# Performance work log

Hardware: AMD Instinct MI355X
Metric: run time of the kernel (lower is better)

The kernel has to match this reference:

```python
import jax, jax.numpy as jnp
import numpy as np

NUM_BITS = 10
MEM_SIZE = 2 ** NUM_BITS  # 1024
HIDDEN = 1024
INPUT = 1024
BATCH = 16384
LN_EPS = 1e-5


def setup_inputs() -> dict:
    key = jax.random.key(0)
    ks = jax.random.split(key, 8)
    s = 0.02
    return {
        "x": jax.random.normal(ks[0], (BATCH, INPUT), jnp.float32),
        "h_prev": jax.random.normal(ks[1], (BATCH, HIDDEN), jnp.float32),
        "memory": jax.random.normal(ks[2], (MEM_SIZE, HIDDEN), jnp.float32),
        "W_w": jax.random.normal(ks[3], (HIDDEN, INPUT), jnp.float32) * s,
        "W_b": jnp.zeros((HIDDEN,), jnp.float32),
        "U_w": jax.random.normal(ks[4], (HIDDEN, HIDDEN), jnp.float32) * s,
        "U_b": jnp.zeros((HIDDEN,), jnp.float32),
        "Q_w": jax.random.normal(ks[5], (HIDDEN, HIDDEN), jnp.float32) * s,
        "Q_b": jnp.zeros((HIDDEN,), jnp.float32),
        "M_w": jax.random.normal(ks[6], (NUM_BITS, HIDDEN), jnp.float32) * s,
        "M_b": jnp.zeros((NUM_BITS,), jnp.float32),
        "ln_g": jnp.ones((HIDDEN,), jnp.float32),
        "ln_b": jnp.zeros((HIDDEN,), jnp.float32),
    }


def reference(x, h_prev, memory, W_w, W_b, U_w, U_b, Q_w, Q_b, M_w, M_b, ln_g, ln_b):
    # Binary address from h_prev (eval-mode hard threshold, non-differentiable)
    powers = jnp.asarray(2 ** np.arange(NUM_BITS - 1, -1, -1), dtype=x.dtype)  # [num_bits]
    logits = h_prev @ M_w.T + M_b                              # [B, num_bits]
    binary = (jax.nn.sigmoid(logits) > 0.5).astype(x.dtype)    # hard bits
    index = jnp.clip((binary * powers).sum(-1).astype(jnp.int32), 0, MEM_SIZE - 1)  # [B]
    h_mem = memory[index]                                      # gather [B, H]
    # Fused linear combine + LayerNorm + sigmoid
    pre = x @ W_w.T + W_b + h_prev @ U_w.T + U_b + h_mem @ Q_w.T + Q_b  # [B, H]
    mu = pre.mean(-1, keepdims=True)
    var = ((pre - mu) ** 2).mean(-1, keepdims=True)            # biased var (torch LN)
    norm = (pre - mu) * jax.lax.rsqrt(var + LN_EPS)
    return jax.nn.sigmoid(norm * ln_g + ln_b)                  # h_new [B, H]
```

## Files before the change

kernel.cpp:

```cpp
#include <hip/hip_runtime.h>

#define BATCH   16384
#define HIDDEN  1024
#define K2      2048
#define MEMSZ   1024
#define NBITS   10

#define BM 256
#define BN 256
#define BK 64
#define NT (K2 / BK)

typedef __bf16 bf16x8 __attribute__((ext_vector_type(8)));
typedef float  f32x4  __attribute__((ext_vector_type(4)));

__device__ __forceinline__ unsigned short f2bf(float f) {
    unsigned int u = __float_as_uint(f);
    u += 0x7FFFu + ((u >> 16) & 1u);
    return (unsigned short)(u >> 16);
}

__device__ __forceinline__ void gload_lds16(const void* g, void* l) {
    __builtin_amdgcn_global_load_lds(
        (const __attribute__((address_space(1))) unsigned int*)g,
        (__attribute__((address_space(3))) unsigned int*)l,
        16, 0, 0);
}

__global__ void pack_kernel(const float* __restrict__ W,
                            const float* __restrict__ U,
                            const float* __restrict__ memory,
                            const float* __restrict__ Q,
                            unsigned short* __restrict__ Bm,
                            unsigned short* __restrict__ Mem,
                            unsigned short* __restrict__ Qb) {
    int u = blockIdx.x * 256 + threadIdx.x;
    const float* src;
    unsigned short* dst;
    if (u < 524288) {
        int n = u >> 9;
        int k = (u & 511) * 4;
        src = (k < 1024) ? (W + (size_t)n * 1024 + k)
                         : (U + (size_t)n * 1024 + (k - 1024));
        dst = Bm + (size_t)n * K2 + k;
    } else if (u < 786432) {
        int f = (u - 524288) * 4;
        src = memory + f;  dst = Mem + f;
    } else if (u < 1048576) {
        int f = (u - 786432) * 4;
        src = Q + f;  dst = Qb + f;
    } else return;
    float4 v = *reinterpret_cast<const float4*>(src);
    ushort4 o;
    o.x = f2bf(v.x); o.y = f2bf(v.y); o.z = f2bf(v.z); o.w = f2bf(v.w);
    *reinterpret_cast<ushort4*>(dst) = o;
}

__global__ __launch_bounds__(256) void mq_kernel(
        const unsigned short* __restrict__ Mem,
        const unsigned short* __restrict__ Qb,
        float* __restrict__ MQ) {
    __shared__ unsigned short As[128 * 64];
    __shared__ unsigned short Bs[128 * 64];

    const int ks = blockIdx.x >> 6;
    const int mb = (blockIdx.x >> 3) & 7;
    const int nb = blockIdx.x & 7;
    const int t    = threadIdx.x;
    const int lane = t & 63;
    const int w    = t >> 6;
    const int wr   = w >> 1, wc = w & 1;
    const int rr   = lane & 15, rq = lane >> 4;
    const int c8   = (t & 7) * 8;
    const int srow = t >> 3;

    f32x4 acc[4][4] = {};

    for (int kt = 0; kt < 4; ++kt) {
        const int k0 = ks * 256 + kt * 64;
#pragma unroll
        for (int i = 0; i < 4; ++i) {
            int r = i * 32 + srow;
            gload_lds16(Mem + (size_t)(mb * 128 + r) * 1024 + k0 + c8, As + i * 2048 + t * 8);
            gload_lds16(Qb  + (size_t)(nb * 128 + r) * 1024 + k0 + c8, Bs + i * 2048 + t * 8);
        }
        __syncthreads();
#pragma unroll
        for (int kk = 0; kk < 2; ++kk) {
            const int krd = kk * 32 + rq * 8;
            bf16x8 af[4], bfv[4];
#pragma unroll
            for (int m = 0; m < 4; ++m)
                af[m] = *reinterpret_cast<const bf16x8*>(As + (wr * 64 + m * 16 + rr) * 64 + krd);
#pragma unroll
            for (int n = 0; n < 4; ++n)
                bfv[n] = *reinterpret_cast<const bf16x8*>(Bs + (wc * 64 + n * 16 + rr) * 64 + krd);
#pragma unroll
            for (int m = 0; m < 4; ++m)
#pragma unroll
                for (int n = 0; n < 4; ++n)
                    acc[m][n] = __builtin_amdgcn_mfma_f32_16x16x32_bf16(
                        af[m], bfv[n], acc[m][n], 0, 0, 0);
        }
        __syncthreads();
    }

#pragma unroll
    for (int m = 0; m < 4; ++m)
#pragma unroll
        for (int n = 0; n < 4; ++n) {
            int gcol = nb * 128 + wc * 64 + n * 16 + rr;
#pragma unroll
            for (int j = 0; j < 4; ++j) {
                int grow = mb * 128 + wr * 64 + m * 16 + rq * 4 + j;
                atomicAdd(&MQ[(size_t)grow * 1024 + gcol], acc[m][n][j]);
            }
        }
}

__global__ __launch_bounds__(256) void build_a_kernel(
        const float* __restrict__ x,
        const float* __restrict__ h_prev,
        const float* __restrict__ M_w,
        const float* __restrict__ M_b,
        unsigned short* __restrict__ A,
        int* __restrict__ idxbuf) {
    int row  = (blockIdx.x * blockDim.x + threadIdx.x) >> 6;
    int lane = threadIdx.x & 63;
    if (row >= BATCH) return;

    const float4* hp = reinterpret_cast<const float4*>(h_prev + (size_t)row * HIDDEN);
    float4 hv[4];
#pragma unroll
    for (int i = 0; i < 4; ++i) hv[i] = hp[i * 64 + lane];

    int idx = 0;
#pragma unroll
    for (int j = 0; j < NBITS; ++j) {
        const float4* mp = reinterpret_cast<const float4*>(M_w + (size_t)j * HIDDEN);
        float s = 0.f;
#pragma unroll
        for (int i = 0; i < 4; ++i) {
            float4 m = mp[i * 64 + lane];
            s += hv[i].x * m.x + hv[i].y * m.y + hv[i].z * m.z + hv[i].w * m.w;
        }
#pragma unroll
        for (int off = 32; off >= 1; off >>= 1) s += __shfl_xor(s, off, 64);
        float logit = s + M_b[j];
        if (logit > 0.f) idx |= (1 << (NBITS - 1 - j));
    }
    if (lane == 0) idxbuf[row] = idx;

    unsigned short* arow = A + (size_t)row * K2;
    const float4* xp = reinterpret_cast<const float4*>(x + (size_t)row * HIDDEN);
#pragma unroll
    for (int i = 0; i < 4; ++i) {
        int off = i * 256 + lane * 4;
        float4 vx = xp[i * 64 + lane];
        ushort4 ox; ox.x = f2bf(vx.x); ox.y = f2bf(vx.y); ox.z = f2bf(vx.z); ox.w = f2bf(vx.w);
        *reinterpret_cast<ushort4*>(arow + off) = ox;

        ushort4 oh; oh.x = f2bf(hv[i].x); oh.y = f2bf(hv[i].y); oh.z = f2bf(hv[i].z); oh.w = f2bf(hv[i].w);
        *reinterpret_cast<ushort4*>(arow + 1024 + off) = oh;
    }
}


__device__ __forceinline__ void stage_g(const unsigned short* __restrict__ src,
                                        int rowbase, int kt, int g,
                                        unsigned short* ldsTile, int t) {
    const int o      = g * 8192 + t * 16;
    const int row    = o >> 7;
    const int inner  = o & 127;
    const int sinner = inner ^ ((row & 7) << 4);
    const char* gp = reinterpret_cast<const char*>(
                         src + (size_t)(rowbase + row) * K2 + kt * BK) + sinner;
    gload_lds16(gp, reinterpret_cast<char*>(ldsTile) + o);
}

__device__ __forceinline__ bf16x8 ldsfrag(const unsigned short* tile, int row,
                                          int kbyte_x_sw) {
    return *reinterpret_cast<const bf16x8*>(
        reinterpret_cast<const char*>(tile) + row * 128 + kbyte_x_sw);
}

#define WAIT_PH(N)                                                   \
    do {                                                             \
        asm volatile("" ::: "memory");                               \
        __builtin_amdgcn_s_barrier();                                \
        asm volatile("s_waitcnt lgkmcnt(" #N ")" ::: "memory");      \
        __builtin_amdgcn_sched_barrier(0);                           \
    } while (0)

#define BAR_OUT()                                                    \
    do {                                                             \
        __builtin_amdgcn_sched_barrier(0);                           \
        asm volatile("" ::: "memory");                               \
        __builtin_amdgcn_s_barrier();                                \
    } while (0)

#define MFMA_Q(AF, MB, NB)                                                     \
    {                                                                          \
        __builtin_amdgcn_s_setprio(1);                                         \
        _Pragma("unroll") for (int m_ = 0; m_ < 4; ++m_)                       \
        _Pragma("unroll") for (int n_ = 0; n_ < 2; ++n_)                       \
        _Pragma("unroll") for (int kk_ = 0; kk_ < 2; ++kk_)                    \
            acc[(MB) + m_][(NB) + n_] =                                        \
                __builtin_amdgcn_mfma_f32_16x16x32_bf16(                       \
                    AF[m_][kk_], bfr[(NB) + n_][kk_],                          \
                    acc[(MB) + m_][(NB) + n_], 0, 0, 0);                       \
        __builtin_amdgcn_s_setprio(0);                                         \
    }

__global__ __launch_bounds__(512, 2) void gemm_kernel(
        const unsigned short* __restrict__ A,
        const unsigned short* __restrict__ Bm,
        float* __restrict__ C) {
    __shared__ alignas(16) unsigned short lds[2][2][BM * BK];

    const int bid  = blockIdx.x;
    const int wgid = (bid & 7) * 32 + (bid >> 3);
    const int mblk = wgid >> 2;
    const int nblk = wgid & 3;

    const int t    = threadIdx.x;
    const int lane = t & 63;
    const int w    = t >> 6;
    const int wr   = w >> 2;
    const int wc   = w & 3;
    const int rr   = lane & 15;
    const int rq   = lane >> 4;
    const int sw   = (rr & 7) << 4;
    const int rqb  = rq * 16;
    const int wrb  = wr * 128;
    const int wcb  = wc * 64;

    const int arow = mblk * BM;
    const int brow = nblk * BN;

    f32x4 acc[8][4] = {};

    {
#pragma unroll
        for (int g = 0; g < 4; ++g) stage_g(A,  arow, 0, g, &lds[0][0][0], t);
#pragma unroll
        for (int g = 0; g < 4; ++g) stage_g(Bm, brow, 0, g, &lds[0][1][0], t);
#pragma unroll
        for (int g = 0; g < 4; ++g) stage_g(Bm, brow, 1, g, &lds[1][1][0], t);
#pragma unroll
        for (int g = 0; g < 2; ++g) stage_g(A,  arow, 1, g, &lds[1][0][0], t);
        asm volatile("s_waitcnt vmcnt(6)" ::: "memory");
        asm volatile("" ::: "memory");
        __builtin_amdgcn_s_barrier();
    }

    bf16x8 af [4][2];
    bf16x8 af2[4][2];
    bf16x8 bfr[4][2];

#pragma unroll
    for (int m = 0; m < 4; ++m) {
        af[m][0] = ldsfrag(&lds[0][0][0], wrb + m * 16 + rr, (rqb) ^ sw);
        af[m][1] = ldsfrag(&lds[0][0][0], wrb + m * 16 + rr, (64 + rqb) ^ sw);
    }
#pragma unroll
    for (int n = 0; n < 2; ++n) {
        bfr[n][0] = ldsfrag(&lds[0][1][0], wcb + n * 16 + rr, (rqb) ^ sw);
        bfr[n][1] = ldsfrag(&lds[0][1][0], wcb + n * 16 + rr, (64 + rqb) ^ sw);
    }

    for (int kt = 0; kt < NT; ++kt) {
        const int c = kt & 1;
        const unsigned short* At = &lds[c][0][0];
        const unsigned short* Bt = &lds[c][1][0];
        const unsigned short* nxA = &lds[c ^ 1][0][0];
        const unsigned short* nxB = &lds[c ^ 1][1][0];
        unsigned short* curA = &lds[c][0][0];
        unsigned short* curB = &lds[c][1][0];
        const bool pf1 = (kt + 1 < NT);
        const bool pf2 = (kt + 2 < NT);

#pragma unroll
        for (int n = 2; n < 4; ++n) {
            bfr[n][0] = ldsfrag(Bt, wcb + n * 16 + rr, (rqb) ^ sw);
            bfr[n][1] = ldsfrag(Bt, wcb + n * 16 + rr, (64 + rqb) ^ sw);
        }
        if (pf1) {
            stage_g(A, arow, kt + 1, 2, (unsigned short*)nxA, t);
            stage_g(A, arow, kt + 1, 3, (unsigned short*)nxA, t);
        }
        WAIT_PH(4);
        MFMA_Q(af, 0, 0);
        BAR_OUT();

#pragma unroll
        for (int m = 0; m < 4; ++m) {
            af2[m][0] = ldsfrag(At, wrb + 64 + m * 16 + rr, (rqb) ^ sw);
            af2[m][1] = ldsfrag(At, wrb + 64 + m * 16 + rr, (64 + rqb) ^ sw);
        }
        WAIT_PH(8);
        MFMA_Q(af, 0, 2);
        BAR_OUT();

        if (pf2) {
            stage_g(Bm, brow, kt + 2, 0, curB, t);
            stage_g(Bm, brow, kt + 2, 1, curB, t);
        }
        WAIT_PH(0);
        MFMA_Q(af2, 4, 0);
        __builtin_amdgcn_sched_barrier(0);
        if (kt < NT - 2) {
            asm volatile("s_waitcnt vmcnt(2)" ::: "memory");
        } else if (kt == NT - 2) {
            asm volatile("s_waitcnt vmcnt(0)" ::: "memory");
        }
        asm volatile("" ::: "memory");
        __builtin_amdgcn_s_barrier();

        if (pf1) {
#pragma unroll
            for (int m = 0; m < 4; ++m) {
                af[m][0] = ldsfrag(nxA, wrb + m * 16 + rr, (rqb) ^ sw);
                af[m][1] = ldsfrag(nxA, wrb + m * 16 + rr, (64 + rqb) ^ sw);
            }
#pragma unroll
            for (int n = 0; n < 2; ++n) {
                bfr[n][0] = ldsfrag(nxB, wcb + n * 16 + rr, (rqb) ^ sw);
                bfr[n][1] = ldsfrag(nxB, wcb + n * 16 + rr, (64 + rqb) ^ sw);
            }
        }
        if (pf2) {
            stage_g(Bm, brow, kt + 2, 2, curB, t);
            stage_g(Bm, brow, kt + 2, 3, curB, t);
            stage_g(A,  arow, kt + 2, 0, curA, t);
            stage_g(A,  arow, kt + 2, 1, curA, t);
        }
        if (pf1) { WAIT_PH(12); } else { WAIT_PH(0); }
        MFMA_Q(af2, 4, 2);
        BAR_OUT();
    }

#pragma unroll
    for (int mi = 0; mi < 8; ++mi) {
#pragma unroll
        for (int n = 0; n < 4; ++n) {
            const int gcol = nblk * BN + wcb + n * 16 + rr;
#pragma unroll
            for (int j = 0; j < 4; ++j) {
                const int grow = mblk * BM + wrb + mi * 16 + rq * 4 + j;
                C[(size_t)grow * HIDDEN + gcol] = acc[mi][n][j];
            }
        }
    }
}

__global__ __launch_bounds__(256) void ln_kernel(
        float* __restrict__ C,
        const int* __restrict__ idxbuf,
        const float* __restrict__ MQ,
        const float* __restrict__ W_b, const float* __restrict__ U_b,
        const float* __restrict__ Q_b, const float* __restrict__ ln_g,
        const float* __restrict__ ln_b) {
    const int row = blockIdx.x;
    const int t   = threadIdx.x;
    const int midx = idxbuf[row];
    float4* rowp = reinterpret_cast<float4*>(C + (size_t)row * HIDDEN);
    const float4* mqp = reinterpret_cast<const float4*>(MQ + (size_t)midx * HIDDEN);

    float4 p  = rowp[t];
    float4 mq = mqp[t];
    float4 bw = reinterpret_cast<const float4*>(W_b)[t];
    float4 bu = reinterpret_cast<const float4*>(U_b)[t];
    float4 bq = reinterpret_cast<const float4*>(Q_b)[t];
    p.x += mq.x + bw.x + bu.x + bq.x;
    p.y += mq.y + bw.y + bu.y + bq.y;
    p.z += mq.z + bw.z + bu.z + bq.z;
    p.w += mq.w + bw.w + bu.w + bq.w;

    float s  = p.x + p.y + p.z + p.w;
    float sq = p.x * p.x + p.y * p.y + p.z * p.z + p.w * p.w;
#pragma unroll
    for (int off = 32; off >= 1; off >>= 1) {
        s  += __shfl_xor(s,  off, 64);
        sq += __shfl_xor(sq, off, 64);
    }
    __shared__ float red[8];
    const int lane = t & 63, w = t >> 6;
    if (lane == 0) { red[w] = s; red[4 + w] = sq; }
    __syncthreads();
    const float S    = red[0] + red[1] + red[2] + red[3];
    const float SQ   = red[4] + red[5] + red[6] + red[7];
    const float mean = S * (1.0f / HIDDEN);
    const float var  = SQ * (1.0f / HIDDEN) - mean * mean;
    const float rstd = rsqrtf(var + 1e-5f);

    float4 g = reinterpret_cast<const float4*>(ln_g)[t];
    float4 b = reinterpret_cast<const float4*>(ln_b)[t];
    float4 o;
    o.x = 1.f / (1.f + __expf(-((p.x - mean) * rstd * g.x + b.x)));
    o.y = 1.f / (1.f + __expf(-((p.y - mean) * rstd * g.y + b.y)));
    o.z = 1.f / (1.f + __expf(-((p.z - mean) * rstd * g.z + b.z)));
    o.w = 1.f / (1.f + __expf(-((p.w - mean) * rstd * g.w + b.w)));
    rowp[t] = o;
}

extern "C" void kernel_launch(void* const* d_in, const int* in_sizes, int n_in,
                              void* d_out, int out_size, void* d_ws, size_t ws_size,
                              hipStream_t stream) {
    const float* x      = (const float*)d_in[0];
    const float* h_prev = (const float*)d_in[1];
    const float* memory = (const float*)d_in[2];
    const float* W_w    = (const float*)d_in[3];
    const float* W_b    = (const float*)d_in[4];
    const float* U_w    = (const float*)d_in[5];
    const float* U_b    = (const float*)d_in[6];
    const float* Q_w    = (const float*)d_in[7];
    const float* Q_b    = (const float*)d_in[8];
    const float* M_w    = (const float*)d_in[9];
    const float* M_b    = (const float*)d_in[10];
    const float* ln_g   = (const float*)d_in[11];
    const float* ln_b   = (const float*)d_in[12];

    char* ws = (char*)d_ws;
    unsigned short* A   = (unsigned short*)(ws);
    unsigned short* Bm  = (unsigned short*)(ws + 67108864);
    unsigned short* Mem = (unsigned short*)(ws + 71303168);
    unsigned short* Qb  = (unsigned short*)(ws + 73400320);
    float*          MQ  = (float*)         (ws + 75497472);
    int*            idx = (int*)           (ws + 79691776);
    float* pre = (float*)d_out;

    hipLaunchKernelGGL(pack_kernel, dim3(4096), dim3(256), 0, stream,
                       W_w, U_w, memory, Q_w, Bm, Mem, Qb);
    hipMemsetAsync(MQ, 0, (size_t)MEMSZ * HIDDEN * sizeof(float), stream);
    hipLaunchKernelGGL(mq_kernel, dim3(256), dim3(256), 0, stream,
                       Mem, Qb, MQ);
    hipLaunchKernelGGL(build_a_kernel, dim3(BATCH / 4), dim3(256), 0, stream,
                       x, h_prev, M_w, M_b, A, idx);
    hipLaunchKernelGGL(gemm_kernel, dim3((BATCH / BM) * (HIDDEN / BN)), dim3(512), 0, stream,
                       A, Bm, pre);
    hipLaunchKernelGGL(ln_kernel, dim3(BATCH), dim3(256), 0, stream,
                       pre, idx, MQ, W_b, U_b, Q_b, ln_g, ln_b);
}
```

Baseline: 170.2 us.

## Merge pack and build kernels; reschedule GEMM LDS prefetch and fragment loads

Fuses the weight-packing kernel and the A-building/address kernel into one launch, with block ranges selecting the role, removing a launch and letting the two phases overlap. Restructures the GEMM main loop so B fragments use two separate register sets and A fragment loads are spread across phases. Full B tiles are now staged early and full A tiles after the third MFMA quadrant, with waitcnt and barrier placement adjusted to match. This trades a different latency-hiding schedule and register pressure for fewer stalls, and risks vmcnt mismatches.

```diff
diff --git a/kernel.cpp b/kernel.cpp
--- a/kernel.cpp
+++ b/kernel.cpp
@@ -27,33 +27,76 @@
         16, 0, 0);
 }
 
-__global__ void pack_kernel(const float* __restrict__ W,
-                            const float* __restrict__ U,
-                            const float* __restrict__ memory,
-                            const float* __restrict__ Q,
-                            unsigned short* __restrict__ Bm,
-                            unsigned short* __restrict__ Mem,
-                            unsigned short* __restrict__ Qb) {
-    int u = blockIdx.x * 256 + threadIdx.x;
-    const float* src;
-    unsigned short* dst;
-    if (u < 524288) {
-        int n = u >> 9;
-        int k = (u & 511) * 4;
-        src = (k < 1024) ? (W + (size_t)n * 1024 + k)
-                         : (U + (size_t)n * 1024 + (k - 1024));
-        dst = Bm + (size_t)n * K2 + k;
-    } else if (u < 786432) {
-        int f = (u - 524288) * 4;
-        src = memory + f;  dst = Mem + f;
-    } else if (u < 1048576) {
-        int f = (u - 786432) * 4;
-        src = Q + f;  dst = Qb + f;
-    } else return;
-    float4 v = *reinterpret_cast<const float4*>(src);
-    ushort4 o;
-    o.x = f2bf(v.x); o.y = f2bf(v.y); o.z = f2bf(v.z); o.w = f2bf(v.w);
-    *reinterpret_cast<ushort4*>(dst) = o;
+__global__ __launch_bounds__(256) void pack_build_kernel(
+        const float* __restrict__ W, const float* __restrict__ U,
+        const float* __restrict__ memory, const float* __restrict__ Q,
+        const float* __restrict__ x, const float* __restrict__ h_prev,
+        const float* __restrict__ M_w, const float* __restrict__ M_b,
+        unsigned short* __restrict__ Bm, unsigned short* __restrict__ Mem,
+        unsigned short* __restrict__ Qb, unsigned short* __restrict__ A,
+        int* __restrict__ idxbuf) {
+    if (blockIdx.x < 4096) {
+        int u = blockIdx.x * 256 + threadIdx.x;
+        const float* src;
+        unsigned short* dst;
+        if (u < 524288) {
+            int n = u >> 9;
+            int k = (u & 511) * 4;
+            src = (k < 1024) ? (W + (size_t)n * 1024 + k)
+                             : (U + (size_t)n * 1024 + (k - 1024));
+            dst = Bm + (size_t)n * K2 + k;
+        } else if (u < 786432) {
+            int f = (u - 524288) * 4;
+            src = memory + f;  dst = Mem + f;
+        } else {
+            int f = (u - 786432) * 4;
+            src = Q + f;  dst = Qb + f;
+        }
+        float4 v = *reinterpret_cast<const float4*>(src);
+        ushort4 o;
+        o.x = f2bf(v.x); o.y = f2bf(v.y); o.z = f2bf(v.z); o.w = f2bf(v.w);
+        *reinterpret_cast<ushort4*>(dst) = o;
+        return;
+    }
+
+    int row  = ((blockIdx.x - 4096) * 256 + threadIdx.x) >> 6;
+    int lane = threadIdx.x & 63;
+    if (row >= BATCH) return;
+
+    const float4* hp = reinterpret_cast<const float4*>(h_prev + (size_t)row * HIDDEN);
+    float4 hv[4];
+#pragma unroll
+    for (int i = 0; i < 4; ++i) hv[i] = hp[i * 64 + lane];
+
+    int idx = 0;
+#pragma unroll
+    for (int j = 0; j < NBITS; ++j) {
+        const float4* mp = reinterpret_cast<const float4*>(M_w + (size_t)j * HIDDEN);
+        float s = 0.f;
+#pragma unroll
+        for (int i = 0; i < 4; ++i) {
+            float4 m = mp[i * 64 + lane];
+            s += hv[i].x * m.x + hv[i].y * m.y + hv[i].z * m.z + hv[i].w * m.w;
+        }
+#pragma unroll
+        for (int off = 32; off >= 1; off >>= 1) s += __shfl_xor(s, off, 64);
+        float logit = s + M_b[j];
+        if (logit > 0.f) idx |= (1 << (NBITS - 1 - j));
+    }
+    if (lane == 0) idxbuf[row] = idx;
+
+    unsigned short* arow = A + (size_t)row * K2;
+    const float4* xp = reinterpret_cast<const float4*>(x + (size_t)row * HIDDEN);
+#pragma unroll
+    for (int i = 0; i < 4; ++i) {
+        int off = i * 256 + lane * 4;
+        float4 vx = xp[i * 64 + lane];
+        ushort4 ox; ox.x = f2bf(vx.x); ox.y = f2bf(vx.y); ox.z = f2bf(vx.z); ox.w = f2bf(vx.w);
+        *reinterpret_cast<ushort4*>(arow + off) = ox;
+
+        ushort4 oh; oh.x = f2bf(hv[i].x); oh.y = f2bf(hv[i].y); oh.z = f2bf(hv[i].z); oh.w = f2bf(hv[i].w);
+        *reinterpret_cast<ushort4*>(arow + 1024 + off) = oh;
+    }
 }
 
 __global__ __launch_bounds__(256) void mq_kernel(
@@ -118,53 +161,6 @@
         }
 }
 
-__global__ __launch_bounds__(256) void build_a_kernel(
-        const float* __restrict__ x,
-        const float* __restrict__ h_prev,
-        const float* __restrict__ M_w,
-        const float* __restrict__ M_b,
-        unsigned short* __restrict__ A,
-        int* __restrict__ idxbuf) {
-    int row  = (blockIdx.x * blockDim.x + threadIdx.x) >> 6;
-    int lane = threadIdx.x & 63;
-    if (row >= BATCH) return;
-
-    const float4* hp = reinterpret_cast<const float4*>(h_prev + (size_t)row * HIDDEN);
-    float4 hv[4];
-#pragma unroll
-    for (int i = 0; i < 4; ++i) hv[i] = hp[i * 64 + lane];
-
-    int idx = 0;
-#pragma unroll
-    for (int j = 0; j < NBITS; ++j) {
-        const float4* mp = reinterpret_cast<const float4*>(M_w + (size_t)j * HIDDEN);
-        float s = 0.f;
-#pragma unroll
-        for (int i = 0; i < 4; ++i) {
-            float4 m = mp[i * 64 + lane];
-            s += hv[i].x * m.x + hv[i].y * m.y + hv[i].z * m.z + hv[i].w * m.w;
-        }
-#pragma unroll
-        for (int off = 32; off >= 1; off >>= 1) s += __shfl_xor(s, off, 64);
-        float logit = s + M_b[j];
-        if (logit > 0.f) idx |= (1 << (NBITS - 1 - j));
-    }
-    if (lane == 0) idxbuf[row] = idx;
-
-    unsigned short* arow = A + (size_t)row * K2;
-    const float4* xp = reinterpret_cast<const float4*>(x + (size_t)row * HIDDEN);
-#pragma unroll
-    for (int i = 0; i < 4; ++i) {
-        int off = i * 256 + lane * 4;
-        float4 vx = xp[i * 64 + lane];
-        ushort4 ox; ox.x = f2bf(vx.x); ox.y = f2bf(vx.y); ox.z = f2bf(vx.z); ox.w = f2bf(vx.w);
-        *reinterpret_cast<ushort4*>(arow + off) = ox;
-
-        ushort4 oh; oh.x = f2bf(hv[i].x); oh.y = f2bf(hv[i].y); oh.z = f2bf(hv[i].z); oh.w = f2bf(hv[i].w);
-        *reinterpret_cast<ushort4*>(arow + 1024 + off) = oh;
-    }
-}
-
 
 __device__ __forceinline__ void stage_g(const unsigned short* __restrict__ src,
                                         int rowbase, int kt, int g,
@@ -199,7 +195,7 @@
         __builtin_amdgcn_s_barrier();                                \
     } while (0)
 
-#define MFMA_Q(AF, MB, NB)                                                     \
+#define MFMA_Q(AF, BF, MB, NB)                                                 \
     {                                                                          \
         __builtin_amdgcn_s_setprio(1);                                         \
         _Pragma("unroll") for (int m_ = 0; m_ < 4; ++m_)                       \
@@ -207,7 +203,7 @@
         _Pragma("unroll") for (int kk_ = 0; kk_ < 2; ++kk_)                    \
             acc[(MB) + m_][(NB) + n_] =                                        \
                 __builtin_amdgcn_mfma_f32_16x16x32_bf16(                       \
-                    AF[m_][kk_], bfr[(NB) + n_][kk_],                          \
+                    AF[m_][kk_], BF[n_][kk_],                                  \
                     acc[(MB) + m_][(NB) + n_], 0, 0, 0);                       \
         __builtin_amdgcn_s_setprio(0);                                         \
     }
@@ -248,15 +244,16 @@
 #pragma unroll
         for (int g = 0; g < 4; ++g) stage_g(Bm, brow, 1, g, &lds[1][1][0], t);
 #pragma unroll
-        for (int g = 0; g < 2; ++g) stage_g(A,  arow, 1, g, &lds[1][0][0], t);
-        asm volatile("s_waitcnt vmcnt(6)" ::: "memory");
+        for (int g = 0; g < 4; ++g) stage_g(A,  arow, 1, g, &lds[1][0][0], t);
+        asm volatile("s_waitcnt vmcnt(8)" ::: "memory");
         asm volatile("" ::: "memory");
         __builtin_amdgcn_s_barrier();
     }
 
-    bf16x8 af [4][2];
-    bf16x8 af2[4][2];
-    bf16x8 bfr[4][2];
+    bf16x8 af  [4][2];
+    bf16x8 af2 [4][2];
+    bf16x8 bfr01[2][2];
+    bf16x8 bfr23[2][2];
 
 #pragma unroll
     for (int m = 0; m < 4; ++m) {
@@ -265,14 +262,15 @@
     }
 #pragma unroll
     for (int n = 0; n < 2; ++n) {
-        bfr[n][0] = ldsfrag(&lds[0][1][0], wcb + n * 16 + rr, (rqb) ^ sw);
-        bfr[n][1] = ldsfrag(&lds[0][1][0], wcb + n * 16 + rr, (64 + rqb) ^ sw);
-    }
+        bfr01[n][0] = ldsfrag(&lds[0][1][0], wcb + n * 16 + rr, (rqb) ^ sw);
+        bfr01[n][1] = ldsfrag(&lds[0][1][0], wcb + n * 16 + rr, (64 + rqb) ^ sw);
+    }
+    __builtin_amdgcn_sched_barrier(0);
 
     for (int kt = 0; kt < NT; ++kt) {
         const int c = kt & 1;
-        const unsigned short* At = &lds[c][0][0];
-        const unsigned short* Bt = &lds[c][1][0];
+        const unsigned short* At  = &lds[c][0][0];
+        const unsigned short* Bt  = &lds[c][1][0];
         const unsigned short* nxA = &lds[c ^ 1][0][0];
         const unsigned short* nxB = &lds[c ^ 1][1][0];
         unsigned short* curA = &lds[c][0][0];
@@ -281,62 +279,65 @@
         const bool pf2 = (kt + 2 < NT);
 
 #pragma unroll
-        for (int n = 2; n < 4; ++n) {
-            bfr[n][0] = ldsfrag(Bt, wcb + n * 16 + rr, (rqb) ^ sw);
-            bfr[n][1] = ldsfrag(Bt, wcb + n * 16 + rr, (64 + rqb) ^ sw);
-        }
-        if (pf1) {
-            stage_g(A, arow, kt + 1, 2, (unsigned short*)nxA, t);
-            stage_g(A, arow, kt + 1, 3, (unsigned short*)nxA, t);
-        }
-        WAIT_PH(4);
-        MFMA_Q(af, 0, 0);
+        for (int n = 0; n < 2; ++n) {
+            bfr23[n][0] = ldsfrag(Bt, wcb + 32 + n * 16 + rr, (rqb) ^ sw);
+            bfr23[n][1] = ldsfrag(Bt, wcb + 32 + n * 16 + rr, (64 + rqb) ^ sw);
+        }
+        __builtin_amdgcn_sched_barrier(0);
+        af2[0][0] = ldsfrag(At, wrb + 64 + rr, (rqb) ^ sw);
+        af2[0][1] = ldsfrag(At, wrb + 64 + rr, (64 + rqb) ^ sw);
+        WAIT_PH(6);
+        MFMA_Q(af, bfr01, 0, 0);
         BAR_OUT();
 
 #pragma unroll
-        for (int m = 0; m < 4; ++m) {
+        for (int m = 1; m < 4; ++m) {
             af2[m][0] = ldsfrag(At, wrb + 64 + m * 16 + rr, (rqb) ^ sw);
             af2[m][1] = ldsfrag(At, wrb + 64 + m * 16 + rr, (64 + rqb) ^ sw);
         }
         WAIT_PH(8);
-        MFMA_Q(af, 0, 2);
-        BAR_OUT();
+        MFMA_Q(af, bfr23, 0, 2);
+        __builtin_amdgcn_sched_barrier(0);
+        asm volatile("s_waitcnt vmcnt(0)" ::: "memory");
+        asm volatile("" ::: "memory");
+        __builtin_amdgcn_s_barrier();
 
         if (pf2) {
             stage_g(Bm, brow, kt + 2, 0, curB, t);
             stage_g(Bm, brow, kt + 2, 1, curB, t);
-        }
-        WAIT_PH(0);
-        MFMA_Q(af2, 4, 0);
-        __builtin_amdgcn_sched_barrier(0);
-        if (kt < NT - 2) {
-            asm volatile("s_waitcnt vmcnt(2)" ::: "memory");
-        } else if (kt == NT - 2) {
-            asm volatile("s_waitcnt vmcnt(0)" ::: "memory");
-        }
-        asm volatile("" ::: "memory");
-        __builtin_amdgcn_s_barrier();
-
+            stage_g(Bm, brow, kt + 2, 2, curB, t);
+            stage_g(Bm, brow, kt + 2, 3, curB, t);
+        }
         if (pf1) {
 #pragma unroll
-            for (int m = 0; m < 4; ++m) {
+            for (int m = 0; m < 3; ++m) {
                 af[m][0] = ldsfrag(nxA, wrb + m * 16 + rr, (rqb) ^ sw);
                 af[m][1] = ldsfrag(nxA, wrb + m * 16 + rr, (64 + rqb) ^ sw);
             }
+            WAIT_PH(6);
+        } else {
+            WAIT_PH(0);
+        }
+        MFMA_Q(af2, bfr01, 4, 0);
+        BAR_OUT();
+
+        if (pf2) {
+            stage_g(A, arow, kt + 2, 0, curA, t);
+            stage_g(A, arow, kt + 2, 1, curA, t);
+            stage_g(A, arow, kt + 2, 2, curA, t);
+            stage_g(A, arow, kt + 2, 3, curA, t);
+        }
+        if (pf1) {
+            af[3][0] = ldsfrag(nxA, wrb + 48 + rr, (rqb) ^ sw);
+            af[3][1] = ldsfrag(nxA, wrb + 48 + rr, (64 + rqb) ^ sw);
 #pragma unroll
             for (int n = 0; n < 2; ++n) {
-                bfr[n][0] = ldsfrag(nxB, wcb + n * 16 + rr, (rqb) ^ sw);
-                bfr[n][1] = ldsfrag(nxB, wcb + n * 16 + rr, (64 + rqb) ^ sw);
+                bfr01[n][0] = ldsfrag(nxB, wcb + n * 16 + rr, (rqb) ^ sw);
+                bfr01[n][1] = ldsfrag(nxB, wcb + n * 16 + rr, (64 + rqb) ^ sw);
             }
         }
-        if (pf2) {
-            stage_g(Bm, brow, kt + 2, 2, curB, t);
-            stage_g(Bm, brow, kt + 2, 3, curB, t);
-            stage_g(A,  arow, kt + 2, 0, curA, t);
-            stage_g(A,  arow, kt + 2, 1, curA, t);
-        }
-        if (pf1) { WAIT_PH(12); } else { WAIT_PH(0); }
-        MFMA_Q(af2, 4, 2);
+        WAIT_PH(12);
+        MFMA_Q(af2, bfr23, 4, 2);
         BAR_OUT();
     }
 
@@ -430,13 +431,12 @@
     int*            idx = (int*)           (ws + 79691776);
     float* pre = (float*)d_out;
 
-    hipLaunchKernelGGL(pack_kernel, dim3(4096), dim3(256), 0, stream,
-                       W_w, U_w, memory, Q_w, Bm, Mem, Qb);
+    hipLaunchKernelGGL(pack_build_kernel, dim3(8192), dim3(256), 0, stream,
+                       W_w, U_w, memory, Q_w, x, h_prev, M_w, M_b,
+                       Bm, Mem, Qb, A, idx);
     hipMemsetAsync(MQ, 0, (size_t)MEMSZ * HIDDEN * sizeof(float), stream);
     hipLaunchKernelGGL(mq_kernel, dim3(256), dim3(256), 0, stream,
                        Mem, Qb, MQ);
-    hipLaunchKernelGGL(build_a_kernel, dim3(BATCH / 4), dim3(256), 0, stream,
-                       x, h_prev, M_w, M_b, A, idx);
     hipLaunchKernelGGL(gemm_kernel, dim3((BATCH / BM) * (HIDDEN / BN)), dim3(512), 0, stream,
                        A, Bm, pre);
     hipLaunchKernelGGL(ln_kernel, dim3(BATCH), dim3(256), 0, stream,
```

Result: faster. 166.6 us (-2.1%).
